# Performance work log

Hardware: AMD Instinct MI355X
Metric: run time of the kernel (lower is better)

Reference implementation:

```python
import jax, jax.numpy as jnp
import numpy as np

D_MODEL = 1024
N_HEADS = 16
DIM_HEAD = D_MODEL // N_HEADS
SCALE = DIM_HEAD ** (-0.5)
B, T = 8, 1024


def setup_inputs() -> dict:
    key = jax.random.key(0)
    k1, k2, k3 = jax.random.split(key, 3)
    x = jax.random.normal(k1, (B, T, D_MODEL), dtype=jnp.float32)
    m = jnp.ones((B, T), dtype=jnp.float32)  # padding mask (1 = keep)
    w_qkv = jax.random.normal(k2, (3 * D_MODEL, D_MODEL), dtype=jnp.float32) * (D_MODEL ** -0.5)
    w_out = jax.random.normal(k3, (D_MODEL, D_MODEL), dtype=jnp.float32) * (D_MODEL ** -0.5)
    b_out = jnp.zeros((D_MODEL,), dtype=jnp.float32)
    return {"x": x, "m": m, "w_qkv": w_qkv, "w_out": w_out, "b_out": b_out, "l": T}


def reference(x, m, w_qkv, w_out, b_out, l):
    b, t, dm = x.shape
    qkv = jnp.einsum('btd,ed->bte', x, w_qkv)  # (b,t,3*d_model)
    q, k, v = jnp.split(qkv, 3, axis=-1)
    rs = lambda a: a.reshape(b, t, N_HEADS, DIM_HEAD)
    q, k, v = rs(q), rs(k), rs(v)
    e = jnp.einsum('bihd,bjhd->bijh', q, k) * SCALE  # (b,i,j,h)
    # combined padding + causal mask
    kpm = m[:, :, None] * m[:, None, :]              # (b,i,j)
    kpm = jnp.tril(kpm)[..., None]                   # (b,i,j,1)
    neg = -jnp.finfo(e.dtype).max
    e = jnp.where(kpm == 0, neg, e)
    a = jax.nn.softmax(e, axis=2)                    # softmax over j
    o = jnp.einsum('bijh,bjhd->bihd', a, v).reshape(b, t, dm)
    o = jnp.einsum('btd,ed->bte', o, w_out) + b_out
    # dropout is identity in eval mode
    return o * m[..., None]
```

## Files before the change

### kernel.cpp

```cpp
#include <hip/hip_runtime.h>
#include <cstdint>
#include <cstddef>

typedef unsigned short u16;
typedef __bf16 bf16;
typedef bf16 __attribute__((ext_vector_type(2))) bf16x2;
typedef bf16 __attribute__((ext_vector_type(8))) bf16x8;
typedef float __attribute__((ext_vector_type(4))) f32x4;
typedef u16 __attribute__((ext_vector_type(8))) u16x8;

#define QSCALE 0.18033688011112042f

__device__ __forceinline__ u16 f2b(float x) {
  unsigned u = __float_as_uint(x);
  unsigned r = (u + 0x7fffu + ((u >> 16) & 1u)) >> 16;
  return (u16)r;
}

__device__ __forceinline__ void gl_lds16(const void* g, void* lds) {
  __builtin_amdgcn_global_load_lds(
      (const __attribute__((address_space(1))) unsigned int*)g,
      (__attribute__((address_space(3))) unsigned int*)lds, 16, 0, 0);
}

__device__ __forceinline__ bf16x8 frag(const u16* base, int row, int kchunk) {
  const int c = kchunk ^ (row & 7);
  return *(const bf16x8*)(base + row * 64 + c * 8);
}
__device__ __forceinline__ void stage_tile4(const u16* gbase, int K, char* lbase,
                                            int wave, int lane) {
#pragma unroll
  for (int i = 0; i < 4; ++i) {
    const int q = wave * 64 + lane + i * 256;
    const int r = q >> 3, c = (q & 7) ^ (r & 7);
    gl_lds16(gbase + (size_t)r * K + c * 8, lbase + i * 4096 + wave * 1024);
  }
}

__device__ __forceinline__ bf16x8 frag32(const u16* base, int row, int kchunk) {
  const int c = kchunk ^ ((row >> 1) & 3);
  return *(const bf16x8*)(base + row * 32 + c * 8);
}
__device__ __forceinline__ void stage32(const u16* gbase, int K, char* lbase,
                                        int wave, int lane) {
  const int q0 = wave * 64 + lane;
  const int r0 = q0 >> 2, c0 = (q0 & 3) ^ ((r0 >> 1) & 3);
  gl_lds16(gbase + (size_t)r0 * K + c0 * 8, lbase + wave * 1024);
  const int q1 = q0 + 256;
  const int r1 = q1 >> 2, c1 = (q1 & 3) ^ ((r1 >> 1) & 3);
  gl_lds16(gbase + (size_t)r1 * K + c1 * 8, lbase + 4096 + wave * 1024);
}

__global__ __launch_bounds__(256) void castk(const float* __restrict__ in,
                                             u16* __restrict__ out, int n) {
  int i = (blockIdx.x * 256 + threadIdx.x) * 8;
  if (i >= n) return;
  float4 a = *(const float4*)(in + i);
  float4 b = *(const float4*)(in + i + 4);
  u16x8 v;
  v[0] = f2b(a.x); v[1] = f2b(a.y); v[2] = f2b(a.z); v[3] = f2b(a.w);
  v[4] = f2b(b.x); v[5] = f2b(b.y); v[6] = f2b(b.z); v[7] = f2b(b.w);
  *(u16x8*)(out + i) = v;
}

__global__ __launch_bounds__(256, 3) void gemm_qkv(
    const u16* __restrict__ A, const u16* __restrict__ B,
    u16* __restrict__ Qo, u16* __restrict__ Ko, u16* __restrict__ Vo) {
  __shared__ u16 As[3][128 * 32];
  __shared__ u16 Bs[3][128 * 32];
  const int tid = threadIdx.x;
  const int lane = tid & 63, wave = tid >> 6;
  const int fr = lane & 15, fg = lane >> 4;
  const int wr = wave >> 1, wc = wave & 1;
  const int bid = blockIdx.x;
  const int bm = bid & 63, bn = bid >> 6;
  const int K = 1024;
  const u16* Ab = A + (size_t)bm * 128 * K;
  const u16* Bb = B + (size_t)bn * 128 * K;

  f32x4 acc[4][4] = {};

  stage32(Ab, K, (char*)&As[0][0], wave, lane);
  stage32(Bb, K, (char*)&Bs[0][0], wave, lane);
  stage32(Ab + 32, K, (char*)&As[1][0], wave, lane);
  stage32(Bb + 32, K, (char*)&Bs[1][0], wave, lane);

  int cur = 0;
#pragma unroll 1
  for (int t = 0; t < 32; ++t) {
    if (t == 31) asm volatile("s_waitcnt vmcnt(0) lgkmcnt(0)" ::: "memory");
    else         asm volatile("s_waitcnt vmcnt(4) lgkmcnt(0)" ::: "memory");
    __builtin_amdgcn_s_barrier();
    __builtin_amdgcn_sched_barrier(0);
    if (t + 2 < 32) {
      int stg = cur + 2; if (stg >= 3) stg -= 3;
      stage32(Ab + (size_t)(t + 2) * 32, K, (char*)&As[stg][0], wave, lane);
      stage32(Bb + (size_t)(t + 2) * 32, K, (char*)&Bs[stg][0], wave, lane);
    }
    bf16x8 af[4], bfv[4];
#pragma unroll
    for (int mi = 0; mi < 4; ++mi)
      af[mi] = frag32(&As[cur][0], wr * 64 + mi * 16 + fr, fg);
#pragma unroll
    for (int ni = 0; ni < 4; ++ni)
      bfv[ni] = frag32(&Bs[cur][0], wc * 64 + ni * 16 + fr, fg);
#pragma unroll
    for (int mi = 0; mi < 4; ++mi)
#pragma unroll
      for (int ni = 0; ni < 4; ++ni)
        acc[mi][ni] = __builtin_amdgcn_mfma_f32_16x16x32_bf16(
            af[mi], bfv[ni], acc[mi][ni], 0, 0, 0);
    cur = (cur + 1 == 3) ? 0 : cur + 1;
  }

  const int gr0 = bm * 128 + wr * 64;
  const int gc0 = bn * 128 + wc * 64;
#pragma unroll
  for (int mi = 0; mi < 4; ++mi) {
    const int rb = gr0 + mi * 16 + fg * 4;
    const int b = rb >> 10, t = rb & 1023;
#pragma unroll
    for (int ni = 0; ni < 4; ++ni) {
      const int c = gc0 + ni * 16 + fr;
      const int region = c >> 10, cc = c & 1023;
      const int h = cc >> 6, d = cc & 63;
      const size_t bh = (size_t)(b * 16 + h);
      if (region == 0) {
#pragma unroll
        for (int g = 0; g < 4; ++g)
          Qo[(bh * 1024 + t + g) * 64 + d] = f2b(acc[mi][ni][g] * QSCALE);
      } else if (region == 1) {
#pragma unroll
        for (int g = 0; g < 4; ++g)
          Ko[(bh * 1024 + t + g) * 64 + d] = f2b(acc[mi][ni][g]);
      } else {
        ushort4 pv;
        pv.x = f2b(acc[mi][ni][0]);
        pv.y = f2b(acc[mi][ni][1]);
        pv.z = f2b(acc[mi][ni][2]);
        pv.w = f2b(acc[mi][ni][3]);
        *(ushort4*)(Vo + (bh * 64 + d) * 1024 + t) = pv;
      }
    }
  }
}

__global__ __launch_bounds__(256) void gemm_bt2(
    const u16* __restrict__ A, const u16* __restrict__ B,
    float* __restrict__ Co, const float* __restrict__ bias,
    const float* __restrict__ msk) {
  __shared__ u16 As[2][128 * 64];
  __shared__ u16 Bs[2][128 * 64];
  const int tid = threadIdx.x;
  const int lane = tid & 63, wave = tid >> 6;
  const int fr = lane & 15, fg = lane >> 4;
  const int wr = wave >> 1, wc = wave & 1;
  const int bid = blockIdx.x;
  const int bm = bid & 63, bn = bid >> 6;
  const int K = 1024, N = 1024;
  const u16* Ab = A + (size_t)bm * 128 * K;
  const u16* Bb = B + (size_t)bn * 128 * K;

  f32x4 acc[4][4] = {};

  stage_tile4(Ab, K, (char*)&As[0][0], wave, lane);
  stage_tile4(Bb, K, (char*)&Bs[0][0], wave, lane);
  __syncthreads();

  int cur = 0;
#pragma unroll 1
  for (int t = 0; t < 16; ++t) {
    if (t < 15) {
      stage_tile4(Ab + (size_t)(t + 1) * 64, K, (char*)&As[cur ^ 1][0], wave, lane);
      stage_tile4(Bb + (size_t)(t + 1) * 64, K, (char*)&Bs[cur ^ 1][0], wave, lane);
    }
    bf16x8 af[4][2], bfv[4][2];
#pragma unroll
    for (int mi = 0; mi < 4; ++mi)
#pragma unroll
      for (int kk = 0; kk < 2; ++kk)
        af[mi][kk] = frag(&As[cur][0], wr * 64 + mi * 16 + fr, kk * 4 + fg);
#pragma unroll
    for (int ni = 0; ni < 4; ++ni)
#pragma unroll
      for (int kk = 0; kk < 2; ++kk)
        bfv[ni][kk] = frag(&Bs[cur][0], wc * 64 + ni * 16 + fr, kk * 4 + fg);
#pragma unroll
    for (int mi = 0; mi < 4; ++mi)
#pragma unroll
      for (int ni = 0; ni < 4; ++ni)
#pragma unroll
        for (int kk = 0; kk < 2; ++kk)
          acc[mi][ni] = __builtin_amdgcn_mfma_f32_16x16x32_bf16(
              af[mi][kk], bfv[ni][kk], acc[mi][ni], 0, 0, 0);
    __syncthreads();
    cur ^= 1;
  }

  const int gr0 = bm * 128 + wr * 64;
  const int gc0 = bn * 128 + wc * 64;
#pragma unroll
  for (int mi = 0; mi < 4; ++mi) {
    const int rb = gr0 + mi * 16 + fg * 4;
#pragma unroll
    for (int ni = 0; ni < 4; ++ni) {
      const int c = gc0 + ni * 16 + fr;
      const float bo = bias[c];
#pragma unroll
      for (int g = 0; g < 4; ++g) {
        const int r = rb + g;
        Co[(size_t)r * N + c] = (acc[mi][ni][g] + bo) * msk[r];
      }
    }
  }
}

__global__ __launch_bounds__(256) void attnk(const u16* __restrict__ Qb,
                                             const u16* __restrict__ Kb,
                                             const u16* __restrict__ Vtb,
                                             const float* __restrict__ msk,
                                             u16* __restrict__ Ob) {
  __shared__ u16 Ks[2][64 * 64];
  __shared__ u16 Vs[2][64 * 64];
  __shared__ float mlds[1024];
  const int tid = threadIdx.x;
  const int lane = tid & 63, wave = tid >> 6;
  const int fr = lane & 15, fg = lane >> 4;
  const int bid = blockIdx.x;
  const int s = bid >> 7;
  const int bh = bid & 127;
  const int b = bh >> 4, h = bh & 15;

  ((float4*)mlds)[tid] = ((const float4*)(msk + (size_t)b * 1024))[tid];

  auto stage = [&](int kb, int buf) {
    const int q0 = wave * 64 + lane;
    const int r0 = q0 >> 3, c0 = (q0 & 7) ^ (r0 & 7);
    gl_lds16(Kb + ((size_t)bh * 1024 + kb * 64 + r0) * 64 + c0 * 8,
             (char*)&Ks[buf][0] + wave * 1024);
    gl_lds16(Vtb + ((size_t)bh * 64 + r0) * 1024 + kb * 64 + c0 * 8,
             (char*)&Vs[buf][0] + wave * 1024);
    const int q1 = q0 + 256;
    const int r1 = q1 >> 3, c1 = (q1 & 7) ^ (r1 & 7);
    gl_lds16(Kb + ((size_t)bh * 1024 + kb * 64 + r1) * 64 + c1 * 8,
             (char*)&Ks[buf][0] + 4096 + wave * 1024);
    gl_lds16(Vtb + ((size_t)bh * 64 + r1) * 1024 + kb * 64 + c1 * 8,
             (char*)&Vs[buf][0] + 4096 + wave * 1024);
  };

  int qw = s * 64 + wave * 16;
  bf16x8 qf[2];
  auto loadQ = [&]() {
#pragma unroll
    for (int kc = 0; kc < 2; ++kc)
      qf[kc] = *(const bf16x8*)(Qb + ((size_t)bh * 1024 + qw + fr) * 64 +
                                kc * 32 + fg * 8);
  };
  loadQ();

  f32x4 o[4] = {};
  float mrun = -3.0e38f, lrun = 0.f;

  auto writeO = [&]() {
    const float inv = 1.0f / lrun;
#pragma unroll
    for (int g = 0; g < 4; ++g) {
      const float invr = __shfl(inv, fg * 4 + g);
      const int q = qw + fg * 4 + g;
#pragma unroll
      for (int dt = 0; dt < 4; ++dt)
        Ob[((size_t)b * 1024 + q) * 1024 + h * 64 + dt * 16 + fr] =
            f2b(o[dt][g] * invr);
    }
  };

  stage(0, 0);

#pragma unroll 1
  for (int it = 0; it <= 16; ++it) {
    __syncthreads();
    if (it < 16) {
      const int nkb = (it + 1 <= s) ? (it + 1) : (it - s);
      stage(nkb, (it + 1) & 1);
    }
    if (it == s + 1) {
      writeO();
      qw = (15 - s) * 64 + wave * 16;
      loadQ();
#pragma unroll
      for (int dt = 0; dt < 4; ++dt) o[dt] = f32x4{0.f, 0.f, 0.f, 0.f};
      mrun = -3.0e38f;
      lrun = 0.f;
    }
    const int kb = (it <= s) ? it : (it - s - 1);
    const u16* Kc = &Ks[it & 1][0];
    const u16* Vc = &Vs[it & 1][0];

    f32x4 st[4];
    const f32x4 z = {0.f, 0.f, 0.f, 0.f};
#pragma unroll
    for (int nt = 0; nt < 4; ++nt) {
      const int krow = nt * 16 + fr;
      const int cb0r = (0 * 4 + fg) ^ (krow & 7);
      const int cb1r = (1 * 4 + fg) ^ (krow & 7);
      const bf16x8 kf0 = *(const bf16x8*)(Kc + krow * 64 + cb0r * 8);
      const bf16x8 kf1 = *(const bf16x8*)(Kc + krow * 64 + cb1r * 8);
      st[nt] = __builtin_amdgcn_mfma_f32_16x16x32_bf16(kf0, qf[0], z, 0, 0, 0);
      st[nt] = __builtin_amdgcn_mfma_f32_16x16x32_bf16(kf1, qf[1], st[nt], 0, 0, 0);
    }

    float kmv[4][4];
#pragma unroll
    for (int nt = 0; nt < 4; ++nt) {
      const float4 km4 = *(const float4*)(&mlds[kb * 64 + nt * 16 + fg * 4]);
      kmv[nt][0] = km4.x; kmv[nt][1] = km4.y; kmv[nt][2] = km4.z; kmv[nt][3] = km4.w;
    }

    if (kb * 64 + 63 > qw) {
      const int q = qw + fr;
#pragma unroll
      for (int nt = 0; nt < 4; ++nt)
#pragma unroll
        for (int g = 0; g < 4; ++g) {
          const int j = kb * 64 + nt * 16 + fg * 4 + g;
          if (j > q) st[nt][g] = -3.0e38f;
        }
    }

    float mx = st[0][0];
#pragma unroll
    for (int nt = 0; nt < 4; ++nt)
#pragma unroll
      for (int g = 0; g < 4; ++g) mx = fmaxf(mx, st[nt][g]);
    mx = fmaxf(mx, __shfl_xor(mx, 16));
    mx = fmaxf(mx, __shfl_xor(mx, 32));
    float nm, sc;
    int doR;
    if (__all(mx <= mrun + 8.f)) {
      nm = mrun; sc = 1.f; doR = 0;
    } else {
      nm = fmaxf(mrun, mx);
      sc = exp2f(mrun - nm);
      mrun = nm; doR = 1;
    }
    float rs = 0.f;
#pragma unroll
    for (int nt = 0; nt < 4; ++nt)
#pragma unroll
      for (int g = 0; g < 4; ++g) {
        const float pq = exp2f(st[nt][g] - nm) * kmv[nt][g];
        st[nt][g] = pq;
        rs += pq;
      }
    rs += __shfl_xor(rs, 16);
    rs += __shfl_xor(rs, 32);
    lrun = doR ? (lrun * sc + rs) : (lrun + rs);

    int pk[4][2];
#pragma unroll
    for (int nt = 0; nt < 4; ++nt)
#pragma unroll
      for (int hh = 0; hh < 2; ++hh) {
        bf16x2 tp;
        tp[0] = (bf16)st[nt][2 * hh];
        tp[1] = (bf16)st[nt][2 * hh + 1];
        pk[nt][hh] = __builtin_bit_cast(int, tp);
      }

    bf16x8 pa[2];
#pragma unroll
    for (int jc = 0; jc < 2; ++jc) {
      int w[4];
#pragma unroll
      for (int e2 = 0; e2 < 4; ++e2) {
        const int sl = fr + ((fg & 1) << 5) + ((e2 & 2) ? 16 : 0);
        const int lo = __shfl(pk[jc * 2 + 0][e2 & 1], sl);
        const int hi = __shfl(pk[jc * 2 + 1][e2 & 1], sl);
        w[e2] = (fg & 2) ? hi : lo;
      }
      int4 wi = {w[0], w[1], w[2], w[3]};
      pa[jc] = __builtin_bit_cast(bf16x8, wi);
    }

    if (doR) {
#pragma unroll
      for (int g = 0; g < 4; ++g) {
        const float scr = __shfl(sc, fg * 4 + g);
#pragma unroll
        for (int dt = 0; dt < 4; ++dt) o[dt][g] *= scr;
      }
    }

#pragma unroll
    for (int jc = 0; jc < 2; ++jc)
#pragma unroll
      for (int dt = 0; dt < 4; ++dt) {
        const int vrow = dt * 16 + fr;
        const int cb = (jc * 4 + fg) ^ (vrow & 7);
        const bf16x8 vf = *(const bf16x8*)(Vc + vrow * 64 + cb * 8);
        o[dt] = __builtin_amdgcn_mfma_f32_16x16x32_bf16(pa[jc], vf, o[dt], 0, 0, 0);
      }
  }

  writeO();
}

extern "C" void kernel_launch(void* const* d_in, const int* in_sizes, int n_in,
                              void* d_out, int out_size, void* d_ws, size_t ws_size,
                              hipStream_t stream) {
  (void)in_sizes; (void)n_in; (void)out_size; (void)ws_size;
  const float* x = (const float*)d_in[0];
  const float* m = (const float*)d_in[1];
  const float* w_qkv = (const float*)d_in[2];
  const float* w_out = (const float*)d_in[3];
  const float* b_out = (const float*)d_in[4];
  float* out = (float*)d_out;

  char* ws = (char*)d_ws;
  const size_t MB = 1u << 20;
  u16* Xb    = (u16*)(ws + 0);
  u16* Wqkvb = (u16*)(ws + 16 * MB);
  u16* Woutb = (u16*)(ws + 22 * MB);
  u16* Qb    = (u16*)(ws + 24 * MB);
  u16* Kb    = (u16*)(ws + 40 * MB);
  u16* Vtb   = (u16*)(ws + 56 * MB);
  u16* Ob    = Xb;

  castk<<<4096, 256, 0, stream>>>(x, Xb, 8 * 1024 * 1024);
  castk<<<1536, 256, 0, stream>>>(w_qkv, Wqkvb, 3072 * 1024);
  castk<<<512, 256, 0, stream>>>(w_out, Woutb, 1024 * 1024);

  gemm_qkv<<<1536, 256, 0, stream>>>(Xb, Wqkvb, Qb, Kb, Vtb);

  attnk<<<1024, 256, 0, stream>>>(Qb, Kb, Vtb, m, Ob);

  gemm_bt2<<<512, 256, 0, stream>>>(Ob, Woutb, out, b_out, m);
}
```

Baseline: 158.3 us.

## Load K and V fragments directly from global memory instead of LDS staging

```diff
diff --git a/kernel.cpp b/kernel.cpp
--- a/kernel.cpp
+++ b/kernel.cpp
@@ -220,8 +220,6 @@
                                              const u16* __restrict__ Vtb,
                                              const float* __restrict__ msk,
                                              u16* __restrict__ Ob) {
-  __shared__ u16 Ks[2][64 * 64];
-  __shared__ u16 Vs[2][64 * 64];
   __shared__ float mlds[1024];
   const int tid = threadIdx.x;
   const int lane = tid & 63, wave = tid >> 6;
@@ -232,21 +230,7 @@
   const int b = bh >> 4, h = bh & 15;
 
   ((float4*)mlds)[tid] = ((const float4*)(msk + (size_t)b * 1024))[tid];
-
-  auto stage = [&](int kb, int buf) {
-    const int q0 = wave * 64 + lane;
-    const int r0 = q0 >> 3, c0 = (q0 & 7) ^ (r0 & 7);
-    gl_lds16(Kb + ((size_t)bh * 1024 + kb * 64 + r0) * 64 + c0 * 8,
-             (char*)&Ks[buf][0] + wave * 1024);
-    gl_lds16(Vtb + ((size_t)bh * 64 + r0) * 1024 + kb * 64 + c0 * 8,
-             (char*)&Vs[buf][0] + wave * 1024);
-    const int q1 = q0 + 256;
-    const int r1 = q1 >> 3, c1 = (q1 & 7) ^ (r1 & 7);
-    gl_lds16(Kb + ((size_t)bh * 1024 + kb * 64 + r1) * 64 + c1 * 8,
-             (char*)&Ks[buf][0] + 4096 + wave * 1024);
-    gl_lds16(Vtb + ((size_t)bh * 64 + r1) * 1024 + kb * 64 + c1 * 8,
-             (char*)&Vs[buf][0] + 4096 + wave * 1024);
-  };
+  __syncthreads();
 
   int qw = s * 64 + wave * 16;
   bf16x8 qf[2];
@@ -274,15 +258,8 @@
     }
   };
 
-  stage(0, 0);
-
 #pragma unroll 1
   for (int it = 0; it <= 16; ++it) {
-    __syncthreads();
-    if (it < 16) {
-      const int nkb = (it + 1 <= s) ? (it + 1) : (it - s);
-      stage(nkb, (it + 1) & 1);
-    }
     if (it == s + 1) {
       writeO();
       qw = (15 - s) * 64 + wave * 16;
@@ -293,21 +270,34 @@
       lrun = 0.f;
     }
     const int kb = (it <= s) ? it : (it - s - 1);
-    const u16* Kc = &Ks[it & 1][0];
-    const u16* Vc = &Vs[it & 1][0];
+    const u16* Kbase = Kb + ((size_t)bh * 1024 + kb * 64) * 64;
+    const u16* Vbase = Vtb + (size_t)bh * 64 * 1024 + kb * 64;
 
     f32x4 st[4];
     const f32x4 z = {0.f, 0.f, 0.f, 0.f};
+    bf16x8 kf0[4], kf1[4];
 #pragma unroll
     for (int nt = 0; nt < 4; ++nt) {
       const int krow = nt * 16 + fr;
-      const int cb0r = (0 * 4 + fg) ^ (krow & 7);
-      const int cb1r = (1 * 4 + fg) ^ (krow & 7);
-      const bf16x8 kf0 = *(const bf16x8*)(Kc + krow * 64 + cb0r * 8);
-      const bf16x8 kf1 = *(const bf16x8*)(Kc + krow * 64 + cb1r * 8);
-      st[nt] = __builtin_amdgcn_mfma_f32_16x16x32_bf16(kf0, qf[0], z, 0, 0, 0);
-      st[nt] = __builtin_amdgcn_mfma_f32_16x16x32_bf16(kf1, qf[1], st[nt], 0, 0, 0);
-    }
+      kf0[nt] = *(const bf16x8*)(Kbase + krow * 64 + fg * 8);
+      kf1[nt] = *(const bf16x8*)(Kbase + krow * 64 + 32 + fg * 8);
+    }
+    __builtin_amdgcn_s_setprio(1);
+#pragma unroll
+    for (int nt = 0; nt < 4; ++nt) {
+      st[nt] = __builtin_amdgcn_mfma_f32_16x16x32_bf16(kf0[nt], qf[0], z, 0, 0, 0);
+      st[nt] = __builtin_amdgcn_mfma_f32_16x16x32_bf16(kf1[nt], qf[1], st[nt], 0, 0, 0);
+    }
+    __builtin_amdgcn_s_setprio(0);
+
+    bf16x8 vf[2][4];
+#pragma unroll
+    for (int jc = 0; jc < 2; ++jc)
+#pragma unroll
+      for (int dt = 0; dt < 4; ++dt) {
+        const int vrow = dt * 16 + fr;
+        vf[jc][dt] = *(const bf16x8*)(Vbase + (size_t)vrow * 1024 + jc * 32 + fg * 8);
+      }
 
     float kmv[4][4];
 #pragma unroll
@@ -391,15 +381,13 @@
       }
     }
 
+    __builtin_amdgcn_s_setprio(1);
 #pragma unroll
     for (int jc = 0; jc < 2; ++jc)
 #pragma unroll
-      for (int dt = 0; dt < 4; ++dt) {
-        const int vrow = dt * 16 + fr;
-        const int cb = (jc * 4 + fg) ^ (vrow & 7);
-        const bf16x8 vf = *(const bf16x8*)(Vc + vrow * 64 + cb * 8);
-        o[dt] = __builtin_amdgcn_mfma_f32_16x16x32_bf16(pa[jc], vf, o[dt], 0, 0, 0);
-      }
+      for (int dt = 0; dt < 4; ++dt)
+        o[dt] = __builtin_amdgcn_mfma_f32_16x16x32_bf16(pa[jc], vf[jc][dt], o[dt], 0, 0, 0);
+    __builtin_amdgcn_s_setprio(0);
   }
 
   writeO();
```

After: 234.6 us. 48.2% more time.
